# Kernel optimization log

Hardware: AMD Instinct MI355X
Metric: run time of the kernel (lower is better)

Reference implementation:

```python
import jax, jax.numpy as jnp
import numpy as np


def setup_inputs() -> dict:
    key = jax.random.key(0)
    kx, ky = jax.random.split(key)
    x = jax.random.normal(kx, (8, 4096, 3), dtype=jnp.float32)
    y = jax.random.normal(ky, (8, 4096, 3), dtype=jnp.float32)
    return {"x": x, "y": y}


def reference(x, y):
    # Mathematically identical to sum((x[:, :, None] - y[:, None, :])**2, -1)
    # but avoids materializing the [B, n, m, 3] diff tensor.
    x2 = jnp.sum(x * x, axis=-1)              # [B, n]
    y2 = jnp.sum(y * y, axis=-1)              # [B, m]
    xy = jnp.einsum('bnd,bmd->bnm', x, y)     # [B, n, m]
    dist = x2[:, :, None] + y2[:, None, :] - 2.0 * xy  # [B, n, m]
    min_dist_xy = jnp.min(dist, axis=2)       # [B, n] nearest y for each x
    min_dist_yx = jnp.min(dist, axis=1)       # [B, m] nearest x for each y
    return jnp.mean(min_dist_xy, axis=1) + jnp.mean(min_dist_yx, axis=1)  # [B]
```

## Files before the change

### kernel.cpp

```cpp
#include <hip/hip_runtime.h>
#include <math.h>

#define BLK 256
#define NX 8
#define XT 2
#define NPTS 4096
#define YLEN 256
#define CCH (NPTS / YLEN)
#define UNITS 65536

__global__ __launch_bounds__(BLK, 2) void chamfer_partial_kernel(
    const float* __restrict__ X, const float* __restrict__ Y,
    float* __restrict__ partial, float* __restrict__ out)
{
  __shared__ float4 sh[YLEN];

  int lin = blockIdx.x;
  int c   = lin % CCH; lin /= CCH;
  int xt  = lin % XT;  lin /= XT;
  int b   = lin & 7;
  int dir = lin >> 3;

  const float* xs = (dir ? Y : X) + b * (NPTS * 3);
  const float* ys = (dir ? X : Y) + b * (NPTS * 3);

  if (blockIdx.x == 0 && threadIdx.x < 8) out[threadIdx.x] = 0.0f;

  {
    int j = threadIdx.x;
    float y0 = ys[(c * YLEN + j) * 3 + 0];
    float y1 = ys[(c * YLEN + j) * 3 + 1];
    float y2 = ys[(c * YLEN + j) * 3 + 2];
    sh[j] = make_float4(y0, y1, y2, 0.5f * (y0 * y0 + y1 * y1 + y2 * y2));
  }
  __syncthreads();

  int x0i = xt * (BLK * NX) + threadIdx.x * NX;
  float xf[NX * 3];
  {
    const float4* xp = reinterpret_cast<const float4*>(xs + x0i * 3);
    #pragma unroll
    for (int i = 0; i < 6; ++i) {
      float4 p = xp[i];
      xf[i * 4 + 0] = p.x; xf[i * 4 + 1] = p.y;
      xf[i * 4 + 2] = p.z; xf[i * 4 + 3] = p.w;
    }
  }
  float n0[NX], n1[NX], n2[NX], x2h[NX], gm[NX];
  #pragma unroll
  for (int k = 0; k < NX; ++k) {
    float a = xf[k * 3 + 0], bb = xf[k * 3 + 1], cc = xf[k * 3 + 2];
    n0[k] = -a; n1[k] = -bb; n2[k] = -cc;
    x2h[k] = 0.5f * (a * a + bb * bb + cc * cc);
    gm[k] = __builtin_inff();
  }

  #pragma unroll 4
  for (int j = 0; j < YLEN; j += 4) {
    float4 p0 = sh[j], p1 = sh[j + 1], p2 = sh[j + 2], p3 = sh[j + 3];
    #pragma unroll
    for (int k = 0; k < NX; ++k) {
      float ga = fmaf(n0[k], p0.x, fmaf(n1[k], p0.y, fmaf(n2[k], p0.z, p0.w)));
      float gb = fmaf(n0[k], p1.x, fmaf(n1[k], p1.y, fmaf(n2[k], p1.z, p1.w)));
      float gc = fmaf(n0[k], p2.x, fmaf(n1[k], p2.y, fmaf(n2[k], p2.z, p2.w)));
      float gd = fmaf(n0[k], p3.x, fmaf(n1[k], p3.y, fmaf(n2[k], p3.z, p3.w)));
      float m  = fminf(fminf(ga, gb), gc);
      gm[k] = fminf(fminf(m, gd), gm[k]);
    }
  }

  float* dst = partial + (size_t)c * UNITS + dir * 32768 + b * 4096 + x0i;
  float4* d4 = reinterpret_cast<float4*>(dst);
  d4[0] = make_float4(2.0f * (x2h[0] + gm[0]), 2.0f * (x2h[1] + gm[1]),
                      2.0f * (x2h[2] + gm[2]), 2.0f * (x2h[3] + gm[3]));
  d4[1] = make_float4(2.0f * (x2h[4] + gm[4]), 2.0f * (x2h[5] + gm[5]),
                      2.0f * (x2h[6] + gm[6]), 2.0f * (x2h[7] + gm[7]));
}

__global__ __launch_bounds__(BLK, 4) void chamfer_reduce_kernel(
    const float* __restrict__ partial, float* __restrict__ out)
{
  int b = blockIdx.x >> 5;
  int s = blockIdx.x & 31;
  int i = s * BLK + threadIdx.x;
  int dir = i >> 12;
  int xi  = i & 4095;
  int unit = dir * 32768 + b * 4096 + xi;
  float v0 = __builtin_inff(), v1 = v0, v2 = v0, v3 = v0;
  float v4 = v0, v5 = v0, v6 = v0, v7 = v0;
  #pragma unroll
  for (int c = 0; c < CCH; c += 8) {
    v0 = fminf(v0, partial[(size_t)(c + 0) * UNITS + unit]);
    v1 = fminf(v1, partial[(size_t)(c + 1) * UNITS + unit]);
    v2 = fminf(v2, partial[(size_t)(c + 2) * UNITS + unit]);
    v3 = fminf(v3, partial[(size_t)(c + 3) * UNITS + unit]);
    v4 = fminf(v4, partial[(size_t)(c + 4) * UNITS + unit]);
    v5 = fminf(v5, partial[(size_t)(c + 5) * UNITS + unit]);
    v6 = fminf(v6, partial[(size_t)(c + 6) * UNITS + unit]);
    v7 = fminf(v7, partial[(size_t)(c + 7) * UNITS + unit]);
  }
  float v = fminf(fminf(fminf(v0, v1), fminf(v2, v3)),
                  fminf(fminf(v4, v5), fminf(v6, v7)));
  #pragma unroll
  for (int off = 32; off > 0; off >>= 1) v += __shfl_down(v, off, 64);
  __shared__ float wsum[BLK / 64];
  if ((threadIdx.x & 63) == 0) wsum[threadIdx.x >> 6] = v;
  __syncthreads();
  if (threadIdx.x == 0) {
    float t = wsum[0] + wsum[1] + wsum[2] + wsum[3];
    atomicAdd(&out[b], t * (1.0f / 4096.0f));
  }
}

__global__ __launch_bounds__(BLK, 2) void chamfer_direct_kernel(
    const float* __restrict__ X, const float* __restrict__ Y,
    float* __restrict__ out)
{
  extern __shared__ float4 shd[];
  int lin = blockIdx.x;
  int xt  = lin & 1;  lin >>= 1;
  int b   = lin & 7;
  int dir = lin >> 3;
  const float* xs = (dir ? Y : X) + b * (NPTS * 3);
  const float* ys = (dir ? X : Y) + b * (NPTS * 3);

  for (int j = threadIdx.x; j < NPTS; j += BLK) {
    float y0 = ys[j * 3 + 0], y1 = ys[j * 3 + 1], y2 = ys[j * 3 + 2];
    shd[j] = make_float4(y0, y1, y2, 0.5f * (y0 * y0 + y1 * y1 + y2 * y2));
  }
  __syncthreads();

  int x0i = xt * (BLK * 8) + threadIdx.x * 8;
  float xf[24];
  const float4* xp = reinterpret_cast<const float4*>(xs + x0i * 3);
  #pragma unroll
  for (int i = 0; i < 6; ++i) {
    float4 p = xp[i];
    xf[i * 4 + 0] = p.x; xf[i * 4 + 1] = p.y;
    xf[i * 4 + 2] = p.z; xf[i * 4 + 3] = p.w;
  }
  float n0[8], n1[8], n2[8], x2h[8], gm[8];
  #pragma unroll
  for (int k = 0; k < 8; ++k) {
    float a = xf[k * 3 + 0], bb = xf[k * 3 + 1], cc = xf[k * 3 + 2];
    n0[k] = -a; n1[k] = -bb; n2[k] = -cc;
    x2h[k] = 0.5f * (a * a + bb * bb + cc * cc);
    gm[k] = __builtin_inff();
  }
  for (int j = 0; j < NPTS; j += 4) {
    float4 p0 = shd[j], p1 = shd[j + 1], p2 = shd[j + 2], p3 = shd[j + 3];
    #pragma unroll
    for (int k = 0; k < 8; ++k) {
      float ga = fmaf(n0[k], p0.x, fmaf(n1[k], p0.y, fmaf(n2[k], p0.z, p0.w)));
      float gb = fmaf(n0[k], p1.x, fmaf(n1[k], p1.y, fmaf(n2[k], p1.z, p1.w)));
      float gc = fmaf(n0[k], p2.x, fmaf(n1[k], p2.y, fmaf(n2[k], p2.z, p2.w)));
      float gd = fmaf(n0[k], p3.x, fmaf(n1[k], p3.y, fmaf(n2[k], p3.z, p3.w)));
      float m  = fminf(fminf(ga, gb), gc);
      gm[k] = fminf(fminf(m, gd), gm[k]);
    }
  }
  float v = 0.0f;
  #pragma unroll
  for (int k = 0; k < 8; ++k) v += 2.0f * (x2h[k] + gm[k]);
  #pragma unroll
  for (int off = 32; off > 0; off >>= 1) v += __shfl_down(v, off, 64);
  __syncthreads();
  float* red = reinterpret_cast<float*>(shd);
  if ((threadIdx.x & 63) == 0) red[threadIdx.x >> 6] = v;
  __syncthreads();
  if (threadIdx.x == 0) {
    float s = red[0] + red[1] + red[2] + red[3];
    atomicAdd(&out[b], s * (1.0f / 4096.0f));
  }
}

__global__ void zero_out_kernel(float* out)
{
  if (threadIdx.x < 8) out[threadIdx.x] = 0.0f;
}

extern "C" void kernel_launch(void* const* d_in, const int* in_sizes, int n_in,
                              void* d_out, int out_size, void* d_ws, size_t ws_size,
                              hipStream_t stream)
{
  const float* X = (const float*)d_in[0];
  const float* Y = (const float*)d_in[1];
  float* out = (float*)d_out;

  if (ws_size >= (size_t)CCH * UNITS * sizeof(float)) {
    chamfer_partial_kernel<<<2 * 8 * XT * CCH, BLK, 0, stream>>>(
        X, Y, (float*)d_ws, out);
    chamfer_reduce_kernel<<<256, BLK, 0, stream>>>((const float*)d_ws, out);
  } else {
    zero_out_kernel<<<1, 64, 0, stream>>>(out);
    chamfer_direct_kernel<<<2 * 8 * 2, BLK, NPTS * sizeof(float4), stream>>>(
        X, Y, out);
  }
}
```

Baseline: 80.71 us.

## Fuse partial and reduce kernels via cooperative launch with grid sync

Merges the partial-min kernel and the reduction kernel into one cooperative kernel that calls a grid-wide sync, after which 16 blocks reduce the partial minima with float4 loads. This removes one kernel launch and its launch gap. In exchange, the final reduction runs on only 16 blocks instead of 256, and the grid barrier adds its own cost. If the cooperative launch fails, the code falls back to the original two-kernel path.

```diff
diff --git a/kernel.cpp b/kernel.cpp
--- a/kernel.cpp
+++ b/kernel.cpp
@@ -1,5 +1,8 @@
 #include <hip/hip_runtime.h>
+#include <hip/hip_cooperative_groups.h>
 #include <math.h>
+
+namespace cg = cooperative_groups;
 
 #define BLK 256
 #define NX 8
@@ -9,23 +12,11 @@
 #define CCH (NPTS / YLEN)
 #define UNITS 65536
 
-__global__ __launch_bounds__(BLK, 2) void chamfer_partial_kernel(
-    const float* __restrict__ X, const float* __restrict__ Y,
-    float* __restrict__ partial, float* __restrict__ out)
-{
-  __shared__ float4 sh[YLEN];
-
-  int lin = blockIdx.x;
-  int c   = lin % CCH; lin /= CCH;
-  int xt  = lin % XT;  lin /= XT;
-  int b   = lin & 7;
-  int dir = lin >> 3;
-
-  const float* xs = (dir ? Y : X) + b * (NPTS * 3);
-  const float* ys = (dir ? X : Y) + b * (NPTS * 3);
-
-  if (blockIdx.x == 0 && threadIdx.x < 8) out[threadIdx.x] = 0.0f;
-
+__device__ __forceinline__ void partial_core(
+    const float* __restrict__ xs, const float* __restrict__ ys,
+    float* __restrict__ partial, float4* sh,
+    int c, int xt, int b, int dir)
+{
   {
     int j = threadIdx.x;
     float y0 = ys[(c * YLEN + j) * 3 + 0];
@@ -77,6 +68,79 @@
                       2.0f * (x2h[6] + gm[6]), 2.0f * (x2h[7] + gm[7]));
 }
 
+__global__ __launch_bounds__(BLK, 2) void chamfer_fused_kernel(
+    const float* __restrict__ X, const float* __restrict__ Y,
+    float* __restrict__ partial, float* __restrict__ out)
+{
+  __shared__ float4 sh[YLEN];
+
+  int lin = blockIdx.x;
+  int c   = lin % CCH; lin /= CCH;
+  int xt  = lin % XT;  lin /= XT;
+  int b   = lin & 7;
+  int dir = lin >> 3;
+
+  const float* xs = (dir ? Y : X) + b * (NPTS * 3);
+  const float* ys = (dir ? X : Y) + b * (NPTS * 3);
+
+  if (blockIdx.x == 0 && threadIdx.x < 8) out[threadIdx.x] = 0.0f;
+
+  partial_core(xs, ys, partial, sh, c, xt, b, dir);
+
+  cg::this_grid().sync();
+
+  if (blockIdx.x >= 16) return;
+
+  int fdir = blockIdx.x >> 3;
+  int fb   = blockIdx.x & 7;
+  int base = fdir * 32768 + fb * 4096 + threadIdx.x * 16;
+  float4 m0 = make_float4(__builtin_inff(), __builtin_inff(),
+                          __builtin_inff(), __builtin_inff());
+  float4 m1 = m0, m2 = m0, m3 = m0;
+  #pragma unroll
+  for (int cc = 0; cc < CCH; ++cc) {
+    const float4* p = reinterpret_cast<const float4*>(
+        partial + (size_t)cc * UNITS + base);
+    float4 a0 = p[0], a1 = p[1], a2 = p[2], a3 = p[3];
+    m0.x = fminf(m0.x, a0.x); m0.y = fminf(m0.y, a0.y);
+    m0.z = fminf(m0.z, a0.z); m0.w = fminf(m0.w, a0.w);
+    m1.x = fminf(m1.x, a1.x); m1.y = fminf(m1.y, a1.y);
+    m1.z = fminf(m1.z, a1.z); m1.w = fminf(m1.w, a1.w);
+    m2.x = fminf(m2.x, a2.x); m2.y = fminf(m2.y, a2.y);
+    m2.z = fminf(m2.z, a2.z); m2.w = fminf(m2.w, a2.w);
+    m3.x = fminf(m3.x, a3.x); m3.y = fminf(m3.y, a3.y);
+    m3.z = fminf(m3.z, a3.z); m3.w = fminf(m3.w, a3.w);
+  }
+  float s = (m0.x + m0.y + m0.z + m0.w) + (m1.x + m1.y + m1.z + m1.w)
+          + (m2.x + m2.y + m2.z + m2.w) + (m3.x + m3.y + m3.z + m3.w);
+  #pragma unroll
+  for (int off = 32; off > 0; off >>= 1) s += __shfl_down(s, off, 64);
+  __syncthreads();
+  float* red = reinterpret_cast<float*>(sh);
+  if ((threadIdx.x & 63) == 0) red[threadIdx.x >> 6] = s;
+  __syncthreads();
+  if (threadIdx.x == 0) {
+    float t = red[0] + red[1] + red[2] + red[3];
+    atomicAdd(&out[fb], t * (1.0f / 4096.0f));
+  }
+}
+
+__global__ __launch_bounds__(BLK, 2) void chamfer_partial_kernel(
+    const float* __restrict__ X, const float* __restrict__ Y,
+    float* __restrict__ partial, float* __restrict__ out)
+{
+  __shared__ float4 sh[YLEN];
+  int lin = blockIdx.x;
+  int c   = lin % CCH; lin /= CCH;
+  int xt  = lin % XT;  lin /= XT;
+  int b   = lin & 7;
+  int dir = lin >> 3;
+  const float* xs = (dir ? Y : X) + b * (NPTS * 3);
+  const float* ys = (dir ? X : Y) + b * (NPTS * 3);
+  if (blockIdx.x == 0 && threadIdx.x < 8) out[threadIdx.x] = 0.0f;
+  partial_core(xs, ys, partial, sh, c, xt, b, dir);
+}
+
 __global__ __launch_bounds__(BLK, 4) void chamfer_reduce_kernel(
     const float* __restrict__ partial, float* __restrict__ out)
 {
@@ -123,13 +187,11 @@
   int dir = lin >> 3;
   const float* xs = (dir ? Y : X) + b * (NPTS * 3);
   const float* ys = (dir ? X : Y) + b * (NPTS * 3);
-
   for (int j = threadIdx.x; j < NPTS; j += BLK) {
     float y0 = ys[j * 3 + 0], y1 = ys[j * 3 + 1], y2 = ys[j * 3 + 2];
     shd[j] = make_float4(y0, y1, y2, 0.5f * (y0 * y0 + y1 * y1 + y2 * y2));
   }
   __syncthreads();
-
   int x0i = xt * (BLK * 8) + threadIdx.x * 8;
   float xf[24];
   const float4* xp = reinterpret_cast<const float4*>(xs + x0i * 3);
@@ -188,9 +250,16 @@
   float* out = (float*)d_out;
 
   if (ws_size >= (size_t)CCH * UNITS * sizeof(float)) {
-    chamfer_partial_kernel<<<2 * 8 * XT * CCH, BLK, 0, stream>>>(
-        X, Y, (float*)d_ws, out);
-    chamfer_reduce_kernel<<<256, BLK, 0, stream>>>((const float*)d_ws, out);
+    float* ws = (float*)d_ws;
+    void* args[] = {(void*)&X, (void*)&Y, (void*)&ws, (void*)&out};
+    hipError_t err = hipLaunchCooperativeKernel(
+        (const void*)chamfer_fused_kernel, dim3(2 * 8 * XT * CCH), dim3(BLK),
+        args, 0, stream);
+    if (err != hipSuccess) {
+      chamfer_partial_kernel<<<2 * 8 * XT * CCH, BLK, 0, stream>>>(
+          X, Y, ws, out);
+      chamfer_reduce_kernel<<<256, BLK, 0, stream>>>(ws, out);
+    }
   } else {
     zero_out_kernel<<<1, 64, 0, stream>>>(out);
     chamfer_direct_kernel<<<2 * 8 * 2, BLK, NPTS * sizeof(float4), stream>>>(
```

Measured after the change: 136.4 us. 69.0% more time.
